# Performance work log

Hardware: AMD Instinct MI355X
Metric: run time of the kernel (lower is better)

Reference implementation:

```python
import jax, jax.numpy as jnp
import numpy as np

N, K, F_DIM, D = 50000, 20, 256, 128


def setup_inputs() -> dict:
    key = jax.random.key(0)
    ks = jax.random.split(key, 8)
    s = 0.05  # small init scale for numerical stability
    return {
        "h": jax.random.normal(ks[0], (N, F_DIM), dtype=jnp.float32),
        "aggregate_neighbors": jax.random.randint(ks[1], (N, K), 0, N),
        "W_past": jax.random.normal(ks[2], (F_DIM, D), dtype=jnp.float32) * s,
        "W": jax.random.normal(ks[3], (2 * D, D), dtype=jnp.float32) * s,
        "W_ih": jax.random.normal(ks[4], (4 * D, D), dtype=jnp.float32) * s,
        "W_hh": jax.random.normal(ks[5], (4 * D, D), dtype=jnp.float32) * s,
        "b_ih": jax.random.normal(ks[6], (4 * D,), dtype=jnp.float32) * s,
        "b_hh": jax.random.normal(ks[7], (4 * D,), dtype=jnp.float32) * s,
    }


def _lstm(seq, W_ih, W_hh, b_ih, b_hh):
    # seq: (N, K, D) batch_first single-layer LSTM; returns final (h_n, c_n), each (N, D)
    n, _, d = seq.shape

    def step(carry, x_t):
        h_t, c_t = carry
        gates = x_t @ W_ih.T + b_ih + h_t @ W_hh.T + b_hh  # (N, 4D)
        i, f, g, o = jnp.split(gates, 4, axis=-1)
        c = jax.nn.sigmoid(f) * c_t + jax.nn.sigmoid(i) * jnp.tanh(g)
        h_new = jax.nn.sigmoid(o) * jnp.tanh(c)
        return (h_new, c), None

    init = (jnp.zeros((n, d), seq.dtype), jnp.zeros((n, d), seq.dtype))
    (h_n, c_n), _ = jax.lax.scan(step, init, jnp.swapaxes(seq, 0, 1))
    return h_n, c_n


def reference(h, aggregate_neighbors, W_past, W, W_ih, W_hh, b_ih, b_hh):
    hp = h @ W_past                      # (N, D) projected features
    seq = hp[aggregate_neighbors]        # (N, K, D) per-node neighbor gather
    h_n, c_n = _lstm(seq, W_ih, W_hh, b_ih, b_hh)
    neigh = jnp.concatenate([hp, h_n], axis=1)  # (N, 2D)
    out = jax.nn.elu(neigh @ W)          # (N, D)
    return out, h_n, c_n
```

## Files before the change

### kernel.cpp

```cpp
#include <hip/hip_runtime.h>

#define NN 50000
#define KSEQ 20
#define HN_OFF 6400000
#define CN_OFF 12800000

using short8 = __attribute__((ext_vector_type(8))) short;
using f32x4  = __attribute__((ext_vector_type(4))) float;

__device__ __forceinline__ unsigned short f2bf(float f) {
    unsigned int u = __float_as_uint(f);
    return (unsigned short)((u + 0x7FFFu + ((u >> 16) & 1u)) >> 16);
}
__device__ __forceinline__ float exp2x(float x) { float r; asm("v_exp_f32 %0, %1" : "=v"(r) : "v"(x)); return r; }
__device__ __forceinline__ float rcpx(float x)  { float r; asm("v_rcp_f32 %0, %1" : "=v"(r) : "v"(x)); return r; }

#define L2E 1.4426950408889634f
__device__ __forceinline__ float sigp(float y)  { return rcpx(1.f + exp2x(y)); }
__device__ __forceinline__ float tanhp(float y) { return fmaf(-2.f, rcpx(1.f + exp2x(y)), 1.f); }

__global__ void prep_kernel(const float* __restrict__ Wp, const float* __restrict__ W,
                            const float* __restrict__ Wih, const float* __restrict__ Whh,
                            const float* __restrict__ bih, const float* __restrict__ bhh,
                            unsigned short* __restrict__ Wih_b, unsigned short* __restrict__ Whh_b,
                            unsigned short* __restrict__ Wpt, unsigned short* __restrict__ Wtt,
                            float* __restrict__ bsum) {
    int tid = blockIdx.x * blockDim.x + threadIdx.x;
    if (tid < 65536) {
        float sc = ((tid >> 14) == 2) ? (2.f * L2E) : (-L2E);
        Wih_b[tid] = f2bf(Wih[tid] * sc); return;
    }
    tid -= 65536;
    if (tid < 65536) {
        float sc = ((tid >> 14) == 2) ? (2.f * L2E) : (-L2E);
        Whh_b[tid] = f2bf(Whh[tid] * sc); return;
    }
    tid -= 65536;
    if (tid < 32768) { int j = tid >> 8, k = tid & 255; Wpt[tid] = f2bf(Wp[k * 128 + j]); return; }
    tid -= 32768;
    if (tid < 32768) { int j = tid >> 8, k = tid & 255; Wtt[tid] = f2bf(W[k * 128 + j]); return; }
    tid -= 32768;
    if (tid < 512) {
        float sc = ((tid >> 7) == 2) ? (2.f * L2E) : (-L2E);
        bsum[tid] = (bih[tid] + bhh[tid]) * sc;
    }
}

__global__ __launch_bounds__(512, 2) void hp_kernel(const float* __restrict__ h,
                                                    const unsigned short* __restrict__ Wpt,
                                                    unsigned short* __restrict__ hp_bf) {
    __shared__ __align__(16) unsigned char smem[32 * 512];
    const int tid = threadIdx.x;
    const int w = tid >> 6, l = tid & 63;
    const int l15 = l & 15, lq = l >> 4;
    const int base = blockIdx.x * 32;

#pragma unroll
    for (int i = 0; i < 4; ++i) {
        int chunk = tid + 512 * i;
        int row = chunk >> 6, kc = chunk & 63;
        int grow = base + row;
        float4 v = make_float4(0.f, 0.f, 0.f, 0.f);
        if (grow < NN) v = *(const float4*)(h + (size_t)grow * 256 + kc * 4);
        ushort4 bv = make_ushort4(f2bf(v.x), f2bf(v.y), f2bf(v.z), f2bf(v.w));
        int off = (row * 512 + kc * 8) ^ ((row & 7) << 4);
        *(ushort4*)(smem + off) = bv;
    }
    __syncthreads();

    const int jb = w * 16 + l15;
    short8 bf[8];
#pragma unroll
    for (int kt = 0; kt < 8; ++kt)
        bf[kt] = *(const short8*)((const unsigned char*)Wpt + jb * 512 + kt * 64 + lq * 16);

    f32x4 acc[2];
    acc[0] = (f32x4){0.f, 0.f, 0.f, 0.f};
    acc[1] = (f32x4){0.f, 0.f, 0.f, 0.f};
#pragma unroll
    for (int kt = 0; kt < 8; ++kt) {
#pragma unroll
        for (int rt = 0; rt < 2; ++rt) {
            int arow = rt * 16 + l15;
            int off = (arow * 512 + kt * 64 + lq * 16) ^ ((arow & 7) << 4);
            short8 a = *(const short8*)(smem + off);
            acc[rt] = __builtin_amdgcn_mfma_f32_16x16x32_bf16(a, bf[kt], acc[rt], 0, 0, 0);
        }
    }
#pragma unroll
    for (int rt = 0; rt < 2; ++rt)
#pragma unroll
        for (int r = 0; r < 4; ++r) {
            int row = rt * 16 + lq * 4 + r;
            int grow = base + row;
            if (grow < NN) hp_bf[(size_t)grow * 128 + w * 16 + l15] = f2bf(acc[rt][r]);
        }
}

__global__ __launch_bounds__(512, 2) void g_kernel(const unsigned short* __restrict__ hp_bf,
                                                   const unsigned short* __restrict__ Wih_b,
                                                   const float* __restrict__ bsum,
                                                   unsigned short* __restrict__ G) {
    __shared__ __align__(16) unsigned char smem[8192];
    const int tid = threadIdx.x;
    const int w = tid >> 6, l = tid & 63;
    const int l15 = l & 15, lq = l >> 4;
    const int base = blockIdx.x * 32;
    const int colj = w * 16 + l15;

    {
        int row = tid >> 4, c = tid & 15;
        int grow = base + row; if (grow >= NN) grow = NN - 1;
        uint4 v = *(const uint4*)((const unsigned char*)hp_bf + (size_t)grow * 256 + c * 16);
        *(uint4*)(smem + ((row * 256 + c * 16) ^ ((row & 7) << 4))) = v;
    }
    __syncthreads();

    short8 bw[4][4];
    float bi[4];
#pragma unroll
    for (int g = 0; g < 4; ++g) {
#pragma unroll
        for (int kt = 0; kt < 4; ++kt)
            bw[g][kt] = *(const short8*)((const unsigned char*)Wih_b + (g * 128 + colj) * 256 + kt * 64 + lq * 16);
        bi[g] = bsum[g * 128 + colj];
    }
    const int off0 = (l15 * 256 + lq * 16) ^ ((l15 & 7) << 4);

    f32x4 acc[4][2];
#pragma unroll
    for (int g = 0; g < 4; ++g) { acc[g][0] = (f32x4){bi[g], bi[g], bi[g], bi[g]}; acc[g][1] = acc[g][0]; }
#pragma unroll
    for (int kt = 0; kt < 4; ++kt)
#pragma unroll
        for (int rt = 0; rt < 2; ++rt) {
            short8 a = *(const short8*)(smem + rt * 4096 + (off0 ^ (kt << 6)));
#pragma unroll
            for (int g = 0; g < 4; ++g)
                acc[g][rt] = __builtin_amdgcn_mfma_f32_16x16x32_bf16(a, bw[g][kt], acc[g][rt], 0, 0, 0);
        }
#pragma unroll
    for (int rt = 0; rt < 2; ++rt)
#pragma unroll
        for (int e = 0; e < 4; ++e) {
            int grow = base + rt * 16 + lq * 4 + e;
            if (grow < NN) {
                ushort4 pk = make_ushort4(f2bf(acc[0][rt][e]), f2bf(acc[1][rt][e]),
                                          f2bf(acc[2][rt][e]), f2bf(acc[3][rt][e]));
                *(ushort4*)(G + (size_t)grow * 512 + colj * 4) = pk;
            }
        }
}

template<int RP>
__device__ __forceinline__ void lstm_step(unsigned char* lds, int t,
    uint2 (&gx)[4], const short8 (&bw)[4][4], f32x4& cst,
    const unsigned char* Gp, const int* __restrict__ aggrow,
    const int off0, const int colj, const int lq, const int hwb, const int hswz,
    const int base, float* __restrict__ out)
{
    constexpr int NP = RP ^ 1;
    f32x4 acc[4];
#pragma unroll
    for (int e = 0; e < 4; ++e) {
        uint2 u = gx[e];
        acc[0][e] = __uint_as_float(u.x << 16);
        acc[1][e] = __uint_as_float(u.x & 0xFFFF0000u);
        acc[2][e] = __uint_as_float(u.y << 16);
        acc[3][e] = __uint_as_float(u.y & 0xFFFF0000u);
    }
    if (t > 0) {
        __builtin_amdgcn_s_setprio(1);
#pragma unroll
        for (int kt = 0; kt < 4; ++kt) {
            short8 a = *(const short8*)(lds + RP * 4096 + (off0 ^ (kt << 6)));
#pragma unroll
            for (int g = 0; g < 4; ++g)
                acc[g] = __builtin_amdgcn_mfma_f32_16x16x32_bf16(a, bw[g][kt], acc[g], 0, 0, 0);
        }
        __builtin_amdgcn_s_setprio(0);
    }
    if (t <= 18) {
        int i0 = aggrow[0 * KSEQ + t + 1];
        int i1 = aggrow[1 * KSEQ + t + 1];
        int i2 = aggrow[2 * KSEQ + t + 1];
        int i3 = aggrow[3 * KSEQ + t + 1];
        gx[0] = *(const uint2*)(Gp + (size_t)i0 * 1024 + colj * 8);
        gx[1] = *(const uint2*)(Gp + (size_t)i1 * 1024 + colj * 8);
        gx[2] = *(const uint2*)(Gp + (size_t)i2 * 1024 + colj * 8);
        gx[3] = *(const uint2*)(Gp + (size_t)i3 * 1024 + colj * 8);
    }
#pragma unroll
    for (int e = 0; e < 4; ++e) {
        float c = fmaf(sigp(acc[1][e]), cst[e], sigp(acc[0][e]) * tanhp(acc[2][e]));
        cst[e] = c;
        float hv = sigp(acc[3][e]) * tanhp((2.f * L2E) * c);
        unsigned pk;
        asm("v_cvt_pk_bf16_f32 %0, %1, %2" : "=v"(pk) : "v"(hv), "v"(hv));
        *(unsigned short*)(lds + NP * 4096 + (((hwb + e * 256) ^ (hswz ^ (e << 4))))) = (unsigned short)pk;
        if (t == KSEQ - 1) {
            int grow = base + lq * 4 + e;
            out[HN_OFF + (size_t)grow * 128 + colj] = hv;
            out[CN_OFF + (size_t)grow * 128 + colj] = c;
        }
    }
    __syncthreads();
}

__global__ __launch_bounds__(512, 4) void lstm_kernel(const unsigned short* __restrict__ hp_bf,
                                                      const int* __restrict__ agg,
                                                      const unsigned short* __restrict__ G,
                                                      const unsigned short* __restrict__ Whh_b,
                                                      const unsigned short* __restrict__ Wtt,
                                                      float* __restrict__ out) {
    __shared__ __align__(16) unsigned char lds[12288];
    const int tid = threadIdx.x;
    const int w = tid >> 6, l = tid & 63;
    const int l15 = l & 15, lq = l >> 4;
    const int base = blockIdx.x * 16;
    const int colj = w * 16 + l15;

    if (tid < 256) {
        int row = tid >> 4, c = tid & 15;
        uint4 v = *(const uint4*)((const unsigned char*)hp_bf + (size_t)(base + row) * 256 + c * 16);
        *(uint4*)(lds + 8192 + ((row * 256 + c * 16) ^ ((row & 7) << 4))) = v;
    }

    short8 bw[4][4];
#pragma unroll
    for (int g = 0; g < 4; ++g)
#pragma unroll
        for (int kt = 0; kt < 4; ++kt)
            bw[g][kt] = *(const short8*)((const unsigned char*)Whh_b + (g * 128 + colj) * 256 + kt * 64 + lq * 16);

    const int off0 = (l15 * 256 + lq * 16) ^ ((l15 & 7) << 4);
    const int hwb = lq * 1024 + colj * 2;
    const int hswz = (lq & 1) << 6;
    const unsigned char* Gp = (const unsigned char*)G;
    const int* aggrow = agg + (size_t)(base + lq * 4) * KSEQ;

    uint2 gx[4];
    {
        int i0 = aggrow[0], i1 = aggrow[KSEQ], i2 = aggrow[2 * KSEQ], i3 = aggrow[3 * KSEQ];
        gx[0] = *(const uint2*)(Gp + (size_t)i0 * 1024 + colj * 8);
        gx[1] = *(const uint2*)(Gp + (size_t)i1 * 1024 + colj * 8);
        gx[2] = *(const uint2*)(Gp + (size_t)i2 * 1024 + colj * 8);
        gx[3] = *(const uint2*)(Gp + (size_t)i3 * 1024 + colj * 8);
    }
    f32x4 cst = (f32x4){0.f, 0.f, 0.f, 0.f};
    __syncthreads();

#pragma unroll 1
    for (int tt = 0; tt < KSEQ; tt += 2) {
        lstm_step<0>(lds, tt,     gx, bw, cst, Gp, aggrow, off0, colj, lq, hwb, hswz, base, out);
        lstm_step<1>(lds, tt + 1, gx, bw, cst, Gp, aggrow, off0, colj, lq, hwb, hswz, base, out);
    }

    short8 bo[8];
#pragma unroll
    for (int kt = 0; kt < 8; ++kt)
        bo[kt] = *(const short8*)((const unsigned char*)Wtt + colj * 512 + kt * 64 + lq * 16);

    f32x4 a2 = (f32x4){0.f, 0.f, 0.f, 0.f};
#pragma unroll
    for (int kt = 0; kt < 4; ++kt) {
        short8 a = *(const short8*)(lds + 8192 + (off0 ^ (kt << 6)));
        a2 = __builtin_amdgcn_mfma_f32_16x16x32_bf16(a, bo[kt], a2, 0, 0, 0);
    }
#pragma unroll
    for (int kt = 0; kt < 4; ++kt) {
        short8 a = *(const short8*)(lds + (off0 ^ (kt << 6)));
        a2 = __builtin_amdgcn_mfma_f32_16x16x32_bf16(a, bo[kt + 4], a2, 0, 0, 0);
    }
#pragma unroll
    for (int e = 0; e < 4; ++e) {
        int grow = base + lq * 4 + e;
        float v = a2[e];
        out[(size_t)grow * 128 + colj] = (v > 0.f) ? v : (exp2x(L2E * v) - 1.f);
    }
}

extern "C" void kernel_launch(void* const* d_in, const int* in_sizes, int n_in,
                              void* d_out, int out_size, void* d_ws, size_t ws_size,
                              hipStream_t stream) {
    (void)in_sizes; (void)n_in; (void)out_size; (void)ws_size;
    const float* h   = (const float*)d_in[0];
    const int*   agg = (const int*)d_in[1];
    const float* Wp  = (const float*)d_in[2];
    const float* W   = (const float*)d_in[3];
    const float* Wih = (const float*)d_in[4];
    const float* Whh = (const float*)d_in[5];
    const float* bih = (const float*)d_in[6];
    const float* bhh = (const float*)d_in[7];
    float* out = (float*)d_out;

    unsigned short* hp_bf = (unsigned short*)d_ws;
    unsigned short* G     = hp_bf + 6400000;
    unsigned short* Wih_b = G + 25600000;
    unsigned short* Whh_b = Wih_b + 65536;
    unsigned short* Wpt   = Whh_b + 65536;
    unsigned short* Wtt   = Wpt + 32768;
    float*          bsum  = (float*)(Wtt + 32768);

    prep_kernel<<<771, 256, 0, stream>>>(Wp, W, Wih, Whh, bih, bhh, Wih_b, Whh_b, Wpt, Wtt, bsum);
    hp_kernel<<<1563, 512, 0, stream>>>(h, Wpt, hp_bf);
    g_kernel<<<1563, 512, 0, stream>>>(hp_bf, Wih_b, bsum, G);
    lstm_kernel<<<3125, 512, 0, stream>>>(hp_bf, agg, G, Whh_b, Wtt, out);
}
```

Baseline: 334.4 us.

## Fuse projection and input-gate kernels; stage neighbor indices in LDS with two-step prefetch

Result: faster. 300.0 us (-10.3%).

```diff
diff --git a/kernel.cpp b/kernel.cpp
--- a/kernel.cpp
+++ b/kernel.cpp
@@ -46,14 +46,18 @@
     }
 }
 
-__global__ __launch_bounds__(512, 2) void hp_kernel(const float* __restrict__ h,
-                                                    const unsigned short* __restrict__ Wpt,
-                                                    unsigned short* __restrict__ hp_bf) {
-    __shared__ __align__(16) unsigned char smem[32 * 512];
+__global__ __launch_bounds__(512, 2) void hp_g_kernel(const float* __restrict__ h,
+                                                      const unsigned short* __restrict__ Wpt,
+                                                      const unsigned short* __restrict__ Wih_b,
+                                                      const float* __restrict__ bsum,
+                                                      unsigned short* __restrict__ hp_bf,
+                                                      unsigned short* __restrict__ G) {
+    __shared__ __align__(16) unsigned char smem[24576];
     const int tid = threadIdx.x;
     const int w = tid >> 6, l = tid & 63;
     const int l15 = l & 15, lq = l >> 4;
     const int base = blockIdx.x * 32;
+    const int colj = w * 16 + l15;
 
 #pragma unroll
     for (int i = 0; i < 4; ++i) {
@@ -68,15 +72,14 @@
     }
     __syncthreads();
 
-    const int jb = w * 16 + l15;
     short8 bf[8];
 #pragma unroll
     for (int kt = 0; kt < 8; ++kt)
-        bf[kt] = *(const short8*)((const unsigned char*)Wpt + jb * 512 + kt * 64 + lq * 16);
+        bf[kt] = *(const short8*)((const unsigned char*)Wpt + colj * 512 + kt * 64 + lq * 16);
 
     f32x4 acc[2];
     acc[0] = (f32x4){0.f, 0.f, 0.f, 0.f};
-    acc[1] = (f32x4){0.f, 0.f, 0.f, 0.f};
+    acc[1] = acc[0];
 #pragma unroll
     for (int kt = 0; kt < 8; ++kt) {
 #pragma unroll
@@ -93,51 +96,34 @@
         for (int r = 0; r < 4; ++r) {
             int row = rt * 16 + lq * 4 + r;
             int grow = base + row;
-            if (grow < NN) hp_bf[(size_t)grow * 128 + w * 16 + l15] = f2bf(acc[rt][r]);
-        }
-}
-
-__global__ __launch_bounds__(512, 2) void g_kernel(const unsigned short* __restrict__ hp_bf,
-                                                   const unsigned short* __restrict__ Wih_b,
-                                                   const float* __restrict__ bsum,
-                                                   unsigned short* __restrict__ G) {
-    __shared__ __align__(16) unsigned char smem[8192];
-    const int tid = threadIdx.x;
-    const int w = tid >> 6, l = tid & 63;
-    const int l15 = l & 15, lq = l >> 4;
-    const int base = blockIdx.x * 32;
-    const int colj = w * 16 + l15;
-
-    {
-        int row = tid >> 4, c = tid & 15;
-        int grow = base + row; if (grow >= NN) grow = NN - 1;
-        uint4 v = *(const uint4*)((const unsigned char*)hp_bf + (size_t)grow * 256 + c * 16);
-        *(uint4*)(smem + ((row * 256 + c * 16) ^ ((row & 7) << 4))) = v;
-    }
-    __syncthreads();
-
-    short8 bw[4][4];
+            unsigned short hb = f2bf(acc[rt][r]);
+            if (grow < NN) hp_bf[(size_t)grow * 128 + colj] = hb;
+            *(unsigned short*)(smem + 16384 + ((row * 256 + colj * 2) ^ ((row & 7) << 4))) = hb;
+        }
+    __syncthreads();
+
+    short8 bw4[4][4];
     float bi[4];
 #pragma unroll
     for (int g = 0; g < 4; ++g) {
 #pragma unroll
         for (int kt = 0; kt < 4; ++kt)
-            bw[g][kt] = *(const short8*)((const unsigned char*)Wih_b + (g * 128 + colj) * 256 + kt * 64 + lq * 16);
+            bw4[g][kt] = *(const short8*)((const unsigned char*)Wih_b + (g * 128 + colj) * 256 + kt * 64 + lq * 16);
         bi[g] = bsum[g * 128 + colj];
     }
     const int off0 = (l15 * 256 + lq * 16) ^ ((l15 & 7) << 4);
 
-    f32x4 acc[4][2];
-#pragma unroll
-    for (int g = 0; g < 4; ++g) { acc[g][0] = (f32x4){bi[g], bi[g], bi[g], bi[g]}; acc[g][1] = acc[g][0]; }
+    f32x4 ag[4][2];
+#pragma unroll
+    for (int g = 0; g < 4; ++g) { ag[g][0] = (f32x4){bi[g], bi[g], bi[g], bi[g]}; ag[g][1] = ag[g][0]; }
 #pragma unroll
     for (int kt = 0; kt < 4; ++kt)
 #pragma unroll
         for (int rt = 0; rt < 2; ++rt) {
-            short8 a = *(const short8*)(smem + rt * 4096 + (off0 ^ (kt << 6)));
+            short8 a = *(const short8*)(smem + 16384 + rt * 4096 + (off0 ^ (kt << 6)));
 #pragma unroll
             for (int g = 0; g < 4; ++g)
-                acc[g][rt] = __builtin_amdgcn_mfma_f32_16x16x32_bf16(a, bw[g][kt], acc[g][rt], 0, 0, 0);
+                ag[g][rt] = __builtin_amdgcn_mfma_f32_16x16x32_bf16(a, bw4[g][kt], ag[g][rt], 0, 0, 0);
         }
 #pragma unroll
     for (int rt = 0; rt < 2; ++rt)
@@ -145,8 +131,8 @@
         for (int e = 0; e < 4; ++e) {
             int grow = base + rt * 16 + lq * 4 + e;
             if (grow < NN) {
-                ushort4 pk = make_ushort4(f2bf(acc[0][rt][e]), f2bf(acc[1][rt][e]),
-                                          f2bf(acc[2][rt][e]), f2bf(acc[3][rt][e]));
+                ushort4 pk = make_ushort4(f2bf(ag[0][rt][e]), f2bf(ag[1][rt][e]),
+                                          f2bf(ag[2][rt][e]), f2bf(ag[3][rt][e]));
                 *(ushort4*)(G + (size_t)grow * 512 + colj * 4) = pk;
             }
         }
@@ -154,8 +140,8 @@
 
 template<int RP>
 __device__ __forceinline__ void lstm_step(unsigned char* lds, int t,
-    uint2 (&gx)[4], const short8 (&bw)[4][4], f32x4& cst,
-    const unsigned char* Gp, const int* __restrict__ aggrow,
+    uint2 (&gx)[2][4], const short8 (&bw)[4][4], f32x4& cst,
+    const unsigned char* Gp, const unsigned cb,
     const int off0, const int colj, const int lq, const int hwb, const int hswz,
     const int base, float* __restrict__ out)
 {
@@ -163,7 +149,7 @@
     f32x4 acc[4];
 #pragma unroll
     for (int e = 0; e < 4; ++e) {
-        uint2 u = gx[e];
+        uint2 u = gx[RP][e];
         acc[0][e] = __uint_as_float(u.x << 16);
         acc[1][e] = __uint_as_float(u.x & 0xFFFF0000u);
         acc[2][e] = __uint_as_float(u.y << 16);
@@ -180,15 +166,12 @@
         }
         __builtin_amdgcn_s_setprio(0);
     }
-    if (t <= 18) {
-        int i0 = aggrow[0 * KSEQ + t + 1];
-        int i1 = aggrow[1 * KSEQ + t + 1];
-        int i2 = aggrow[2 * KSEQ + t + 1];
-        int i3 = aggrow[3 * KSEQ + t + 1];
-        gx[0] = *(const uint2*)(Gp + (size_t)i0 * 1024 + colj * 8);
-        gx[1] = *(const uint2*)(Gp + (size_t)i1 * 1024 + colj * 8);
-        gx[2] = *(const uint2*)(Gp + (size_t)i2 * 1024 + colj * 8);
-        gx[3] = *(const uint2*)(Gp + (size_t)i3 * 1024 + colj * 8);
+    if (t <= 17) {
+#pragma unroll
+        for (int e = 0; e < 4; ++e) {
+            int idx = *(const int*)(lds + 12288 + (lq * 4 + e) * 80 + (t + 2) * 4);
+            gx[RP][e] = *(const uint2*)(Gp + (((unsigned)idx << 10) + cb));
+        }
     }
 #pragma unroll
     for (int e = 0; e < 4; ++e) {
@@ -197,7 +180,7 @@
         float hv = sigp(acc[3][e]) * tanhp((2.f * L2E) * c);
         unsigned pk;
         asm("v_cvt_pk_bf16_f32 %0, %1, %2" : "=v"(pk) : "v"(hv), "v"(hv));
-        *(unsigned short*)(lds + NP * 4096 + (((hwb + e * 256) ^ (hswz ^ (e << 4))))) = (unsigned short)pk;
+        *(unsigned short*)(lds + NP * 4096 + ((hwb + e * 256) ^ (hswz ^ (e << 4)))) = (unsigned short)pk;
         if (t == KSEQ - 1) {
             int grow = base + lq * 4 + e;
             out[HN_OFF + (size_t)grow * 128 + colj] = hv;
@@ -213,7 +196,7 @@
                                                       const unsigned short* __restrict__ Whh_b,
                                                       const unsigned short* __restrict__ Wtt,
                                                       float* __restrict__ out) {
-    __shared__ __align__(16) unsigned char lds[12288];
+    __shared__ __align__(16) unsigned char lds[14336];
     const int tid = threadIdx.x;
     const int w = tid >> 6, l = tid & 63;
     const int l15 = l & 15, lq = l >> 4;
@@ -225,6 +208,9 @@
         uint4 v = *(const uint4*)((const unsigned char*)hp_bf + (size_t)(base + row) * 256 + c * 16);
         *(uint4*)(lds + 8192 + ((row * 256 + c * 16) ^ ((row & 7) << 4))) = v;
     }
+    if (tid < 320) {
+        *(int*)(lds + 12288 + tid * 4) = agg[(size_t)base * KSEQ + tid];
+    }
 
     short8 bw[4][4];
 #pragma unroll
@@ -237,23 +223,24 @@
     const int hwb = lq * 1024 + colj * 2;
     const int hswz = (lq & 1) << 6;
     const unsigned char* Gp = (const unsigned char*)G;
-    const int* aggrow = agg + (size_t)(base + lq * 4) * KSEQ;
-
-    uint2 gx[4];
-    {
-        int i0 = aggrow[0], i1 = aggrow[KSEQ], i2 = aggrow[2 * KSEQ], i3 = aggrow[3 * KSEQ];
-        gx[0] = *(const uint2*)(Gp + (size_t)i0 * 1024 + colj * 8);
-        gx[1] = *(const uint2*)(Gp + (size_t)i1 * 1024 + colj * 8);
-        gx[2] = *(const uint2*)(Gp + (size_t)i2 * 1024 + colj * 8);
-        gx[3] = *(const uint2*)(Gp + (size_t)i3 * 1024 + colj * 8);
-    }
+    const unsigned cb = (unsigned)colj * 8;
+
     f32x4 cst = (f32x4){0.f, 0.f, 0.f, 0.f};
     __syncthreads();
+
+    uint2 gx[2][4];
+#pragma unroll
+    for (int tp = 0; tp < 2; ++tp)
+#pragma unroll
+        for (int e = 0; e < 4; ++e) {
+            int idx = *(const int*)(lds + 12288 + (lq * 4 + e) * 80 + tp * 4);
+            gx[tp][e] = *(const uint2*)(Gp + (((unsigned)idx << 10) + cb));
+        }
 
 #pragma unroll 1
     for (int tt = 0; tt < KSEQ; tt += 2) {
-        lstm_step<0>(lds, tt,     gx, bw, cst, Gp, aggrow, off0, colj, lq, hwb, hswz, base, out);
-        lstm_step<1>(lds, tt + 1, gx, bw, cst, Gp, aggrow, off0, colj, lq, hwb, hswz, base, out);
+        lstm_step<0>(lds, tt,     gx, bw, cst, Gp, cb, off0, colj, lq, hwb, hswz, base, out);
+        lstm_step<1>(lds, tt + 1, gx, bw, cst, Gp, cb, off0, colj, lq, hwb, hswz, base, out);
     }
 
     short8 bo[8];
@@ -303,7 +290,6 @@
     float*          bsum  = (float*)(Wtt + 32768);
 
     prep_kernel<<<771, 256, 0, stream>>>(Wp, W, Wih, Whh, bih, bhh, Wih_b, Whh_b, Wpt, Wtt, bsum);
-    hp_kernel<<<1563, 512, 0, stream>>>(h, Wpt, hp_bf);
-    g_kernel<<<1563, 512, 0, stream>>>(hp_bf, Wih_b, bsum, G);
+    hp_g_kernel<<<1563, 512, 0, stream>>>(h, Wpt, Wih_b, bsum, hp_bf, G);
     lstm_kernel<<<3125, 512, 0, stream>>>(hp_bf, agg, G, Whh_b, Wtt, out);
 }
```
